# Optimization experiments

Measured on AMD Instinct MI355X. Metric: run time of the kernel, lower is better.

The kernel has to match this reference:

```python
import jax, jax.numpy as jnp
import numpy as np

N_NODES = 50000
N_EDGES = 400000
F_IN = 1024
F_HID = 512
N_GEN = 1024  # nodes flagged as generators (x[:,0] == 1)


def setup_inputs() -> dict:
    key = jax.random.key(0)
    k1, k2, k3, k4 = jax.random.split(key, 4)
    x = jax.random.normal(k1, (N_NODES, F_IN), dtype=jnp.float32)
    x = x.at[:N_GEN, 0].set(1.0)  # generator mask hits exactly these nodes
    edge_index = jax.random.randint(k2, (2, N_EDGES), 0, N_NODES, dtype=jnp.int64)
    # Glorot-ish init for GCN linear weights
    W1 = jax.random.normal(k3, (F_IN, F_HID), dtype=jnp.float32) * (1.0 / np.sqrt(F_IN))
    b1 = jnp.zeros((F_HID,), dtype=jnp.float32)
    W2 = jax.random.normal(k4, (F_HID, 1), dtype=jnp.float32) * (1.0 / np.sqrt(F_HID))
    b2 = jnp.zeros((1,), dtype=jnp.float32)
    return {"x": x, "edge_index": edge_index, "W1": W1, "b1": b1, "W2": W2, "b2": b2}


def _gcn_aggregate(h, src, tgt, dinv_sqrt, n):
    # symmetric-normalized neighbor aggregation with implicit self-loops
    norm = dinv_sqrt[src] * dinv_sqrt[tgt]            # [E]
    agg = jax.ops.segment_sum(norm[:, None] * h[src], tgt, num_segments=n)
    # self-loop term: d_i^{-1/2} * d_i^{-1/2} * h_i
    return agg + h * (dinv_sqrt * dinv_sqrt)[:, None]


def reference(x, edge_index, W1, b1, W2, b2):
    n = x.shape[0]
    src, tgt = edge_index[0], edge_index[1]
    # degrees of A_hat = A + I (in-degree at target + 1 self-loop)
    deg = jax.ops.segment_sum(jnp.ones_like(src, dtype=x.dtype), tgt, num_segments=n) + 1.0
    dinv_sqrt = jax.lax.rsqrt(deg)
    # conv1: transform then aggregate (GCNConv)
    h = _gcn_aggregate(x @ W1, src, tgt, dinv_sqrt, n) + b1
    h = jax.nn.relu(h)
    # dropout is identity in eval mode
    # conv2
    out = _gcn_aggregate(h @ W2, src, tgt, dinv_sqrt, n) + b2   # [N, 1]
    mask = x[:, 0] == 1.0
    # masked generator outputs (full-length vector, zero where not generator)
    return jnp.where(mask, out[:, 0], 0.0)
```

## Files before the change

### kernel.cpp

```cpp
#include <hip/hip_runtime.h>

#define FIN 1024
#define FH  512
#define BM  128
#define BN  128
#define BK  32

typedef __attribute__((ext_vector_type(8))) short short8;
typedef __attribute__((ext_vector_type(4))) float f32x4;
typedef __attribute__((address_space(1))) void gvoid;
typedef __attribute__((address_space(3))) void lvoid;

static __device__ __forceinline__ unsigned short f2bf(float f) {
    unsigned u = __float_as_uint(f);
    unsigned r = (u + 0x7FFFu + ((u >> 16) & 1u)) >> 16;
    return (unsigned short)r;
}
static __device__ __forceinline__ float bf2f(unsigned short h) {
    return __uint_as_float((unsigned)h << 16);
}

__global__ void k_deg(const int* __restrict__ tgt, int E, int* __restrict__ deg) {
    int e = blockIdx.x * blockDim.x + threadIdx.x;
    if (e < E) atomicAdd(&deg[tgt[e]], 1);
}

__global__ void k_node(const float* __restrict__ x, const int* __restrict__ deg,
                       float* __restrict__ dinv, int* __restrict__ mask,
                       int* __restrict__ flag1, int N) {
    int i = blockIdx.x * blockDim.x + threadIdx.x;
    if (i >= N) return;
    dinv[i] = rsqrtf((float)deg[i] + 1.0f);
    int m = (x[(size_t)i * FIN] == 1.0f) ? 1 : 0;
    mask[i]  = m;
    flag1[i] = m;
}

__global__ void k_edge_flag(const int* __restrict__ src, const int* __restrict__ tgt,
                            int E, const int* __restrict__ mask, int* __restrict__ flag1) {
    int e = blockIdx.x * blockDim.x + threadIdx.x;
    if (e < E) {
        if (mask[tgt[e]]) flag1[src[e]] = 1;
    }
}

__global__ void k_acnt(const int* __restrict__ tgt, int E, const int* __restrict__ flag1,
                       int* __restrict__ acnt) {
    int e = blockIdx.x * blockDim.x + threadIdx.x;
    if (e < E) {
        int t = tgt[e];
        if (flag1[t]) atomicAdd(&acnt[t], 1);
    }
}

__global__ void k_base(const int* __restrict__ flag1, const int* __restrict__ acnt,
                       int* __restrict__ aoff, int* __restrict__ list,
                       int* __restrict__ cnts , int N) {
    int i = blockIdx.x * blockDim.x + threadIdx.x;
    if (i >= N) return;
    if (flag1[i]) {
        int idx = atomicAdd(&cnts[1], 1);
        list[idx] = i;
    }
    if (acnt[i] > 0) aoff[i] = atomicAdd(&cnts[0], acnt[i]);
}

__global__ void k_fill(const int* __restrict__ src, const int* __restrict__ tgt, int E,
                       const int* __restrict__ flag1, const int* __restrict__ aoff,
                       int* __restrict__ cur, int* __restrict__ csr_src) {
    int e = blockIdx.x * blockDim.x + threadIdx.x;
    if (e < E) {
        int t = tgt[e];
        if (flag1[t]) {
            int pos = aoff[t] + atomicAdd(&cur[t], 1);
            csr_src[pos] = src[e];
        }
    }
}

__global__ void k_cvt_w1(const float* __restrict__ W1, unsigned short* __restrict__ th,
                         unsigned short* __restrict__ tl) {
    int idx = blockIdx.x * blockDim.x + threadIdx.x;
    if (idx >= FIN * FH) return;
    int k = idx / FH, n = idx % FH;
    float v = W1[idx];
    unsigned short h = f2bf(v);
    unsigned short l = f2bf(v - bf2f(h));
    th[(size_t)n * FIN + k] = h;
    tl[(size_t)n * FIN + k] = l;
}

__global__ __launch_bounds__(256) void k_gemm(const float* __restrict__ Axf,
                                              const unsigned short* __restrict__ Bh,
                                              const unsigned short* __restrict__ Bl,
                                              float* __restrict__ C, int M) {
    __shared__ unsigned short sAh[BM * BK], sAl[BM * BK], sBh[BN * BK], sBl[BN * BK];
    const int tid  = threadIdx.x;
    const int lane = tid & 63;
    const int wid  = tid >> 6;
    const int wm   = wid & 1, wn = wid >> 1;
    const int bm   = blockIdx.y * BM, bn = blockIdx.x * BN;
    const int mlim = M - bm;

    const float* pA = Axf + (size_t)bm * FIN;
    const unsigned short* pBh = Bh + (size_t)bn * FIN;
    const unsigned short* pBl = Bl + (size_t)bn * FIN;

    const int s_kc  = (tid & 3) * 8;
    const int a_row = tid >> 3;
    const int a_kc  = (tid & 7) * 4;

    f32x4 acc[4][4];
    #pragma unroll
    for (int i = 0; i < 4; ++i)
        #pragma unroll
        for (int j = 0; j < 4; ++j)
            #pragma unroll
            for (int r = 0; r < 4; ++r) acc[i][j][r] = 0.f;

#define STAGE_B(S, G)                                                                 \
    __builtin_amdgcn_global_load_lds(                                                 \
        (gvoid*)((G) + (size_t)(tid >> 2) * FIN + k0 + s_kc),                         \
        (lvoid*)((S) + (tid & ~63) * 8), 16, 0, 0);                                   \
    __builtin_amdgcn_global_load_lds(                                                 \
        (gvoid*)((G) + (size_t)(64 + (tid >> 2)) * FIN + k0 + s_kc),                  \
        (lvoid*)((S) + 2048 + (tid & ~63) * 8), 16, 0, 0);

    const int fa = (wm * 64 + (lane & 15)) * BK + (lane >> 4) * 8;
    const int fb = (wn * 64 + (lane & 15)) * BK + (lane >> 4) * 8;

    for (int k0 = 0; k0 < FIN; k0 += BK) {
        float4 av[4];
        #pragma unroll
        for (int r = 0; r < 4; ++r) {
            int row = r * 32 + a_row;
            av[r] = make_float4(0.f, 0.f, 0.f, 0.f);
            if (row < mlim)
                av[r] = *(const float4*)&pA[(size_t)row * FIN + k0 + a_kc];
        }
        STAGE_B(sBh, pBh)
        STAGE_B(sBl, pBl)
        #pragma unroll
        for (int r = 0; r < 4; ++r) {
            int row = r * 32 + a_row;
            ushort4 h, l;
            h.x = f2bf(av[r].x); l.x = f2bf(av[r].x - bf2f(h.x));
            h.y = f2bf(av[r].y); l.y = f2bf(av[r].y - bf2f(h.y));
            h.z = f2bf(av[r].z); l.z = f2bf(av[r].z - bf2f(h.z));
            h.w = f2bf(av[r].w); l.w = f2bf(av[r].w - bf2f(h.w));
            *(ushort4*)&sAh[row * BK + a_kc] = h;
            *(ushort4*)&sAl[row * BK + a_kc] = l;
        }
        __syncthreads();

        short8 ah[4], al[4], bh[4], bl[4];
        #pragma unroll
        for (int i = 0; i < 4; ++i) {
            ah[i] = *(const short8*)&sAh[fa + i * 16 * BK];
            al[i] = *(const short8*)&sAl[fa + i * 16 * BK];
            bh[i] = *(const short8*)&sBh[fb + i * 16 * BK];
            bl[i] = *(const short8*)&sBl[fb + i * 16 * BK];
        }
        #pragma unroll
        for (int i = 0; i < 4; ++i)
            #pragma unroll
            for (int j = 0; j < 4; ++j) {
                acc[i][j] = __builtin_amdgcn_mfma_f32_16x16x32_bf16(ah[i], bh[j], acc[i][j], 0, 0, 0);
                acc[i][j] = __builtin_amdgcn_mfma_f32_16x16x32_bf16(ah[i], bl[j], acc[i][j], 0, 0, 0);
                acc[i][j] = __builtin_amdgcn_mfma_f32_16x16x32_bf16(al[i], bh[j], acc[i][j], 0, 0, 0);
            }
        __syncthreads();
    }
#undef STAGE_B

    #pragma unroll
    for (int i = 0; i < 4; ++i) {
        int row0 = bm + wm * 64 + i * 16 + (lane >> 4) * 4;
        #pragma unroll
        for (int r = 0; r < 4; ++r) {
            int row = row0 + r;
            if (row < M) {
                float* cp = C + (size_t)row * FH + bn + wn * 64 + (lane & 15);
                #pragma unroll
                for (int j = 0; j < 4; ++j) cp[j * 16] = acc[i][j][r];
            }
        }
    }
}

__global__ void k_gather(const int* __restrict__ list, const int* __restrict__ cnts,
                         const int* __restrict__ aoff, const int* __restrict__ acnt,
                         const int* __restrict__ csr_src,
                         const float* __restrict__ dinv, const float* __restrict__ h0,
                         const float* __restrict__ b1, const float* __restrict__ W2,
                         float* __restrict__ sval) {
    int wave = (blockIdx.x * blockDim.x + threadIdx.x) >> 6;
    int lane = threadIdx.x & 63;
    int nw   = (gridDim.x * blockDim.x) >> 6;
    const int nf = cnts[1];
    const float4* b1v = (const float4*)b1;
    const float4* w2v = (const float4*)W2;
    for (int w = wave; w < nf; w += nw) {
        int t = list[w];
        float dt = dinv[t];
        float4 a0 = make_float4(0.f, 0.f, 0.f, 0.f), a1 = a0;
        int n = acnt[t];
        if (n > 0) {
            int start = aoff[t];
            for (int e = 0; e < n; ++e) {
                int s = csr_src[start + e];
                float norm = dinv[s] * dt;
                const float4* hv = (const float4*)(h0 + (size_t)s * FH);
                float4 v0 = hv[lane], v1 = hv[lane + 64];
                a0.x = fmaf(v0.x, norm, a0.x); a0.y = fmaf(v0.y, norm, a0.y);
                a0.z = fmaf(v0.z, norm, a0.z); a0.w = fmaf(v0.w, norm, a0.w);
                a1.x = fmaf(v1.x, norm, a1.x); a1.y = fmaf(v1.y, norm, a1.y);
                a1.z = fmaf(v1.z, norm, a1.z); a1.w = fmaf(v1.w, norm, a1.w);
            }
        }
        float d2 = dt * dt;
        const float4* ht = (const float4*)(h0 + (size_t)t * FH);
        float4 h0t0 = ht[lane],  h0t1 = ht[lane + 64];
        float4 bb0  = b1v[lane], bb1  = b1v[lane + 64];
        float4 w0   = w2v[lane], w1   = w2v[lane + 64];
        float local =
            fmaxf(fmaf(h0t0.x, d2, a0.x) + bb0.x, 0.f) * w0.x +
            fmaxf(fmaf(h0t0.y, d2, a0.y) + bb0.y, 0.f) * w0.y +
            fmaxf(fmaf(h0t0.z, d2, a0.z) + bb0.z, 0.f) * w0.z +
            fmaxf(fmaf(h0t0.w, d2, a0.w) + bb0.w, 0.f) * w0.w +
            fmaxf(fmaf(h0t1.x, d2, a1.x) + bb1.x, 0.f) * w1.x +
            fmaxf(fmaf(h0t1.y, d2, a1.y) + bb1.y, 0.f) * w1.y +
            fmaxf(fmaf(h0t1.z, d2, a1.z) + bb1.z, 0.f) * w1.z +
            fmaxf(fmaf(h0t1.w, d2, a1.w) + bb1.w, 0.f) * w1.w;
        #pragma unroll
        for (int off2 = 32; off2 > 0; off2 >>= 1) local += __shfl_xor(local, off2);
        if (lane == 0) sval[t] = local;
    }
}

__global__ void k_agg2(const int* __restrict__ src, const int* __restrict__ tgt, int E,
                       const int* __restrict__ mask, const float* __restrict__ dinv,
                       const float* __restrict__ sval, float* __restrict__ outacc) {
    int e = blockIdx.x * blockDim.x + threadIdx.x;
    if (e < E) {
        int t = tgt[e];
        if (mask[t]) {
            int s = src[e];
            atomicAdd(&outacc[t], dinv[s] * dinv[t] * sval[s]);
        }
    }
}

__global__ void k_out(const int* __restrict__ mask, const float* __restrict__ outacc,
                      const float* __restrict__ sval, const float* __restrict__ dinv,
                      const float* __restrict__ b2, float* __restrict__ out, int N) {
    int i = blockIdx.x * blockDim.x + threadIdx.x;
    if (i >= N) return;
    float v = 0.f;
    if (mask[i]) v = outacc[i] + sval[i] * dinv[i] * dinv[i] + b2[0];
    out[i] = v;
}

extern "C" void kernel_launch(void* const* d_in, const int* in_sizes, int n_in,
                              void* d_out, int out_size, void* d_ws, size_t ws_size,
                              hipStream_t stream) {
    const float* x  = (const float*)d_in[0];
    const int*   ei = (const int*)d_in[1];
    const float* W1 = (const float*)d_in[2];
    const float* b1 = (const float*)d_in[3];
    const float* W2 = (const float*)d_in[4];
    const float* b2 = (const float*)d_in[5];

    const int N = in_sizes[0] / FIN;
    const int E = in_sizes[1] / 2;
    const int* srcA = ei;
    const int* tgtA = ei + E;

    char* w = (char*)d_ws;
    size_t off = 0;
    auto alloc = [&](size_t b) { char* p = w + off; off += (b + 255) & ~(size_t)255; return p; };
    size_t zoff0 = off;
    int*   deg    = (int*)  alloc((size_t)N * 4);
    int*   acnt   = (int*)  alloc((size_t)N * 4);
    int*   cur    = (int*)  alloc((size_t)N * 4);
    float* outacc = (float*)alloc((size_t)N * 4);
    int*   cnts   = (int*)  alloc(256);
    size_t zbytes = off - zoff0;
    float* dinv   = (float*)alloc((size_t)N * 4);
    int*   mask   = (int*)  alloc((size_t)N * 4);
    int*   flag1  = (int*)  alloc((size_t)N * 4);
    float* sval   = (float*)alloc((size_t)N * 4);
    int*   aoff   = (int*)  alloc((size_t)N * 4);
    int*   list   = (int*)  alloc((size_t)N * 4);
    int*   csrs   = (int*)  alloc((size_t)E * 4);
    float* h0     = (float*)alloc((size_t)N * FH * 4);
    unsigned short* w1th = (unsigned short*)alloc((size_t)FIN * FH * 2);
    unsigned short* w1tl = (unsigned short*)alloc((size_t)FIN * FH * 2);

    hipMemsetAsync(w + zoff0, 0, zbytes, stream);

    k_deg<<<(E + 255) / 256, 256, 0, stream>>>(tgtA, E, deg);
    k_node<<<(N + 255) / 256, 256, 0, stream>>>(x, deg, dinv, mask, flag1, N);
    k_edge_flag<<<(E + 255) / 256, 256, 0, stream>>>(srcA, tgtA, E, mask, flag1);

    k_acnt<<<(E + 255) / 256, 256, 0, stream>>>(tgtA, E, flag1, acnt);
    k_base<<<(N + 255) / 256, 256, 0, stream>>>(flag1, acnt, aoff, list, cnts, N);
    k_fill<<<(E + 255) / 256, 256, 0, stream>>>(srcA, tgtA, E, flag1, aoff, cur, csrs);

    k_cvt_w1<<<(FIN * FH + 255) / 256, 256, 0, stream>>>(W1, w1th, w1tl);

    dim3 gg(FH / BN, (N + BM - 1) / BM);
    k_gemm<<<gg, 256, 0, stream>>>(x, w1th, w1tl, h0, N);

    k_gather<<<2048, 256, 0, stream>>>(list, cnts, aoff, acnt, csrs, dinv, h0, b1, W2, sval);
    k_agg2<<<(E + 255) / 256, 256, 0, stream>>>(srcA, tgtA, E, mask, dinv, sval, outacc);
    k_out<<<(N + 255) / 256, 256, 0, stream>>>(mask, outacc, sval, dinv, b2, (float*)d_out, N);
}
```

Baseline: 558.6 us.

## Double-buffer GEMM LDS tiles, fuse degree counting, tile W1 transpose

The GEMM now double-buffers its LDS tiles. The next A tile is loaded into registers and the next B tile is staged into LDS while MFMAs run on the current tile, and the bf16 hi/lo split is written after compute, which leaves one barrier per iteration. Degree counting is merged into the acnt edge pass and the dinv computation moves into k_base, removing a kernel launch and a full pass over the edges. The W1 split/transpose kernel uses a 32x32 shared-memory tile so its global writes are coalesced. The cost is twice the LDS per block, which may lower occupancy, plus more live registers.

```diff
diff --git a/kernel.cpp b/kernel.cpp
--- a/kernel.cpp
+++ b/kernel.cpp
@@ -5,6 +5,7 @@
 #define BM  128
 #define BN  128
 #define BK  32
+#define NT  (FIN / BK)
 
 typedef __attribute__((ext_vector_type(8))) short short8;
 typedef __attribute__((ext_vector_type(4))) float f32x4;
@@ -20,17 +21,10 @@
     return __uint_as_float((unsigned)h << 16);
 }
 
-__global__ void k_deg(const int* __restrict__ tgt, int E, int* __restrict__ deg) {
-    int e = blockIdx.x * blockDim.x + threadIdx.x;
-    if (e < E) atomicAdd(&deg[tgt[e]], 1);
-}
-
-__global__ void k_node(const float* __restrict__ x, const int* __restrict__ deg,
-                       float* __restrict__ dinv, int* __restrict__ mask,
+__global__ void k_mask(const float* __restrict__ x, int* __restrict__ mask,
                        int* __restrict__ flag1, int N) {
     int i = blockIdx.x * blockDim.x + threadIdx.x;
     if (i >= N) return;
-    dinv[i] = rsqrtf((float)deg[i] + 1.0f);
     int m = (x[(size_t)i * FIN] == 1.0f) ? 1 : 0;
     mask[i]  = m;
     flag1[i] = m;
@@ -44,20 +38,23 @@
     }
 }
 
-__global__ void k_acnt(const int* __restrict__ tgt, int E, const int* __restrict__ flag1,
-                       int* __restrict__ acnt) {
+__global__ void k_deg_acnt(const int* __restrict__ tgt, int E, const int* __restrict__ flag1,
+                           int* __restrict__ deg, int* __restrict__ acnt) {
     int e = blockIdx.x * blockDim.x + threadIdx.x;
     if (e < E) {
         int t = tgt[e];
+        atomicAdd(&deg[t], 1);
         if (flag1[t]) atomicAdd(&acnt[t], 1);
     }
 }
 
-__global__ void k_base(const int* __restrict__ flag1, const int* __restrict__ acnt,
+__global__ void k_base(const int* __restrict__ flag1, const int* __restrict__ deg,
+                       const int* __restrict__ acnt, float* __restrict__ dinv,
                        int* __restrict__ aoff, int* __restrict__ list,
                        int* __restrict__ cnts , int N) {
     int i = blockIdx.x * blockDim.x + threadIdx.x;
     if (i >= N) return;
+    dinv[i] = rsqrtf((float)deg[i] + 1.0f);
     if (flag1[i]) {
         int idx = atomicAdd(&cnts[1], 1);
         list[idx] = i;
@@ -78,23 +75,34 @@
     }
 }
 
-__global__ void k_cvt_w1(const float* __restrict__ W1, unsigned short* __restrict__ th,
-                         unsigned short* __restrict__ tl) {
-    int idx = blockIdx.x * blockDim.x + threadIdx.x;
-    if (idx >= FIN * FH) return;
-    int k = idx / FH, n = idx % FH;
-    float v = W1[idx];
-    unsigned short h = f2bf(v);
-    unsigned short l = f2bf(v - bf2f(h));
-    th[(size_t)n * FIN + k] = h;
-    tl[(size_t)n * FIN + k] = l;
+__global__ __launch_bounds__(256) void k_cvt_w1(const float* __restrict__ W1,
+                                                unsigned short* __restrict__ th,
+                                                unsigned short* __restrict__ tl) {
+    __shared__ float tile[32][33];
+    const int nb = blockIdx.x * 32;
+    const int kb = blockIdx.y * 32;
+    const int tx = threadIdx.x & 31, ty = threadIdx.x >> 5;
+    #pragma unroll
+    for (int r = 0; r < 4; ++r)
+        tile[ty + r * 8][tx] = W1[(size_t)(kb + ty + r * 8) * FH + nb + tx];
+    __syncthreads();
+    #pragma unroll
+    for (int r = 0; r < 4; ++r) {
+        int n = nb + ty + r * 8;
+        float v = tile[tx][ty + r * 8];
+        unsigned short h = f2bf(v);
+        unsigned short l = f2bf(v - bf2f(h));
+        th[(size_t)n * FIN + kb + tx] = h;
+        tl[(size_t)n * FIN + kb + tx] = l;
+    }
 }
 
 __global__ __launch_bounds__(256) void k_gemm(const float* __restrict__ Axf,
                                               const unsigned short* __restrict__ Bh,
                                               const unsigned short* __restrict__ Bl,
                                               float* __restrict__ C, int M) {
-    __shared__ unsigned short sAh[BM * BK], sAl[BM * BK], sBh[BN * BK], sBl[BN * BK];
+    __shared__ unsigned short sAh[2][BM * BK], sAl[2][BM * BK],
+                              sBh[2][BN * BK], sBl[2][BN * BK];
     const int tid  = threadIdx.x;
     const int lane = tid & 63;
     const int wid  = tid >> 6;
@@ -118,48 +126,61 @@
             #pragma unroll
             for (int r = 0; r < 4; ++r) acc[i][j][r] = 0.f;
 
-#define STAGE_B(S, G)                                                                 \
+#define STAGE_B(S, G, K0)                                                             \
     __builtin_amdgcn_global_load_lds(                                                 \
-        (gvoid*)((G) + (size_t)(tid >> 2) * FIN + k0 + s_kc),                         \
+        (gvoid*)((G) + (size_t)(tid >> 2) * FIN + (K0) + s_kc),                       \
         (lvoid*)((S) + (tid & ~63) * 8), 16, 0, 0);                                   \
     __builtin_amdgcn_global_load_lds(                                                 \
-        (gvoid*)((G) + (size_t)(64 + (tid >> 2)) * FIN + k0 + s_kc),                  \
+        (gvoid*)((G) + (size_t)(64 + (tid >> 2)) * FIN + (K0) + s_kc),                \
         (lvoid*)((S) + 2048 + (tid & ~63) * 8), 16, 0, 0);
+
+#define LOAD_A(AV, K0)                                                                \
+    _Pragma("unroll")                                                                 \
+    for (int r = 0; r < 4; ++r) {                                                     \
+        int row_ = r * 32 + a_row;                                                    \
+        AV[r] = make_float4(0.f, 0.f, 0.f, 0.f);                                      \
+        if (row_ < mlim)                                                              \
+            AV[r] = *(const float4*)&pA[(size_t)row_ * FIN + (K0) + a_kc];            \
+    }
+
+#define SPLIT_A(SH, SL, AV)                                                           \
+    _Pragma("unroll")                                                                 \
+    for (int r = 0; r < 4; ++r) {                                                     \
+        int row_ = r * 32 + a_row;                                                    \
+        ushort4 h_, l_;                                                               \
+        h_.x = f2bf(AV[r].x); l_.x = f2bf(AV[r].x - bf2f(h_.x));                      \
+        h_.y = f2bf(AV[r].y); l_.y = f2bf(AV[r].y - bf2f(h_.y));                      \
+        h_.z = f2bf(AV[r].z); l_.z = f2bf(AV[r].z - bf2f(h_.z));                      \
+        h_.w = f2bf(AV[r].w); l_.w = f2bf(AV[r].w - bf2f(h_.w));                      \
+        *(ushort4*)&(SH)[row_ * BK + a_kc] = h_;                                      \
+        *(ushort4*)&(SL)[row_ * BK + a_kc] = l_;                                      \
+    }
 
     const int fa = (wm * 64 + (lane & 15)) * BK + (lane >> 4) * 8;
     const int fb = (wn * 64 + (lane & 15)) * BK + (lane >> 4) * 8;
 
-    for (int k0 = 0; k0 < FIN; k0 += BK) {
-        float4 av[4];
-        #pragma unroll
-        for (int r = 0; r < 4; ++r) {
-            int row = r * 32 + a_row;
-            av[r] = make_float4(0.f, 0.f, 0.f, 0.f);
-            if (row < mlim)
-                av[r] = *(const float4*)&pA[(size_t)row * FIN + k0 + a_kc];
-        }
-        STAGE_B(sBh, pBh)
-        STAGE_B(sBl, pBl)
-        #pragma unroll
-        for (int r = 0; r < 4; ++r) {
-            int row = r * 32 + a_row;
-            ushort4 h, l;
-            h.x = f2bf(av[r].x); l.x = f2bf(av[r].x - bf2f(h.x));
-            h.y = f2bf(av[r].y); l.y = f2bf(av[r].y - bf2f(h.y));
-            h.z = f2bf(av[r].z); l.z = f2bf(av[r].z - bf2f(h.z));
-            h.w = f2bf(av[r].w); l.w = f2bf(av[r].w - bf2f(h.w));
-            *(ushort4*)&sAh[row * BK + a_kc] = h;
-            *(ushort4*)&sAl[row * BK + a_kc] = l;
-        }
-        __syncthreads();
-
+    float4 av[4];
+    LOAD_A(av, 0)
+    STAGE_B(sBh[0], pBh, 0)
+    STAGE_B(sBl[0], pBl, 0)
+    SPLIT_A(sAh[0], sAl[0], av)
+    __syncthreads();
+
+    for (int t = 0; t < NT; ++t) {
+        const int cur = t & 1, nxt = cur ^ 1;
+        const int k1 = (t + 1) * BK;
+        if (t + 1 < NT) {
+            LOAD_A(av, k1)
+            STAGE_B(sBh[nxt], pBh, k1)
+            STAGE_B(sBl[nxt], pBl, k1)
+        }
         short8 ah[4], al[4], bh[4], bl[4];
         #pragma unroll
         for (int i = 0; i < 4; ++i) {
-            ah[i] = *(const short8*)&sAh[fa + i * 16 * BK];
-            al[i] = *(const short8*)&sAl[fa + i * 16 * BK];
-            bh[i] = *(const short8*)&sBh[fb + i * 16 * BK];
-            bl[i] = *(const short8*)&sBl[fb + i * 16 * BK];
+            ah[i] = *(const short8*)&sAh[cur][fa + i * 16 * BK];
+            al[i] = *(const short8*)&sAl[cur][fa + i * 16 * BK];
+            bh[i] = *(const short8*)&sBh[cur][fb + i * 16 * BK];
+            bl[i] = *(const short8*)&sBl[cur][fb + i * 16 * BK];
         }
         #pragma unroll
         for (int i = 0; i < 4; ++i)
@@ -169,9 +190,13 @@
                 acc[i][j] = __builtin_amdgcn_mfma_f32_16x16x32_bf16(ah[i], bl[j], acc[i][j], 0, 0, 0);
                 acc[i][j] = __builtin_amdgcn_mfma_f32_16x16x32_bf16(al[i], bh[j], acc[i][j], 0, 0, 0);
             }
+        if (t + 1 < NT)
+            SPLIT_A(sAh[nxt], sAl[nxt], av)
         __syncthreads();
     }
 #undef STAGE_B
+#undef LOAD_A
+#undef SPLIT_A
 
     #pragma unroll
     for (int i = 0; i < 4; ++i) {
@@ -299,15 +324,14 @@
 
     hipMemsetAsync(w + zoff0, 0, zbytes, stream);
 
-    k_deg<<<(E + 255) / 256, 256, 0, stream>>>(tgtA, E, deg);
-    k_node<<<(N + 255) / 256, 256, 0, stream>>>(x, deg, dinv, mask, flag1, N);
+    k_mask<<<(N + 255) / 256, 256, 0, stream>>>(x, mask, flag1, N);
     k_edge_flag<<<(E + 255) / 256, 256, 0, stream>>>(srcA, tgtA, E, mask, flag1);
-
-    k_acnt<<<(E + 255) / 256, 256, 0, stream>>>(tgtA, E, flag1, acnt);
-    k_base<<<(N + 255) / 256, 256, 0, stream>>>(flag1, acnt, aoff, list, cnts, N);
+    k_deg_acnt<<<(E + 255) / 256, 256, 0, stream>>>(tgtA, E, flag1, deg, acnt);
+    k_base<<<(N + 255) / 256, 256, 0, stream>>>(flag1, deg, acnt, dinv, aoff, list, cnts, N);
     k_fill<<<(E + 255) / 256, 256, 0, stream>>>(srcA, tgtA, E, flag1, aoff, cur, csrs);
 
-    k_cvt_w1<<<(FIN * FH + 255) / 256, 256, 0, stream>>>(W1, w1th, w1tl);
+    dim3 gw(FH / 32, FIN / 32);
+    k_cvt_w1<<<gw, 256, 0, stream>>>(W1, w1th, w1tl);
 
     dim3 gg(FH / BN, (N + BM - 1) / BM);
     k_gemm<<<gg, 256, 0, stream>>>(x, w1th, w1tl, h0, N);
```

Result: no change. 553.9 us (-0.8%).
